# Kernel tuning notes

Measured on AMD Instinct MI355X. Metric: run time of the kernel, lower is better.

Reference implementation:

```python
import jax, jax.numpy as jnp
import numpy as np

N_NODES = 100000
N_EDGES = 3200000
F_IN = 128
NOUT = 32


def _lin(x, W, b):
    return x @ W + b


def _spect_conv(x, src, dst, W, b, n_nodes):
    # edge_attr is all-ones with a single frequency (K=1), so SpectConv reduces to
    # an unweighted scatter-add of linearly transformed source-node features.
    h = x @ W                                   # [N, nout]
    agg = jax.ops.segment_sum(h[src], dst, num_segments=n_nodes)  # [N, nout]
    return agg + b


def setup_inputs() -> dict:
    key = jax.random.key(0)
    ks = jax.random.split(key, 32)
    s = 0.05

    def w(k, shape):
        return jax.random.normal(k, shape, dtype=jnp.float32) * s

    inp = {
        "x": jax.random.normal(ks[0], (N_NODES, F_IN), dtype=jnp.float32),
        "edge_index": jax.random.randint(ks[1], (2, N_EDGES), 0, N_NODES, dtype=jnp.int32),
        # SpectConv weights (single frequency) + biases
        "Wc1": w(ks[2], (F_IN, NOUT)), "bc1": jnp.zeros((NOUT,), jnp.float32),
        "Wc2": w(ks[3], (NOUT, NOUT)), "bc2": jnp.zeros((NOUT,), jnp.float32),
        "Wc3": w(ks[4], (NOUT, NOUT)), "bc3": jnp.zeros((NOUT,), jnp.float32),
        # dense branch weights
        "W11": w(ks[5], (F_IN, NOUT)), "b11": w(ks[6], (NOUT,)),
        "W12": w(ks[7], (F_IN, NOUT)), "b12": w(ks[8], (NOUT,)),
        "W13": w(ks[9], (F_IN, NOUT)), "b13": w(ks[10], (NOUT,)),
        "W21": w(ks[11], (NOUT, NOUT)), "b21": w(ks[12], (NOUT,)),
        "W22": w(ks[13], (NOUT, NOUT)), "b22": w(ks[14], (NOUT,)),
        "W23": w(ks[15], (NOUT, NOUT)), "b23": w(ks[16], (NOUT,)),
        "W31": w(ks[17], (NOUT, NOUT)), "b31": w(ks[18], (NOUT,)),
        "W32": w(ks[19], (NOUT, NOUT)), "b32": w(ks[20], (NOUT,)),
        "W33": w(ks[21], (NOUT, NOUT)), "b33": w(ks[22], (NOUT,)),
        "W2": w(ks[23], (NOUT, 1)), "b2": w(ks[24], (1,)),
    }
    return inp


def reference(x, edge_index,
              Wc1, bc1, Wc2, bc2, Wc3, bc3,
              W11, b11, W12, b12, W13, b13,
              W21, b21, W22, b22, W23, b23,
              W31, b31, W32, b32, W33, b33,
              W2, b2):
    src, dst = edge_index[0], edge_index[1]
    n = x.shape[0]
    relu = jax.nn.relu

    def block(h, Wa, ba, Wc, bc, Wm1, bm1, Wm2, bm2):
        return (relu(_lin(h, Wa, ba))
                + relu(_spect_conv(h, src, dst, Wc, bc, n))
                + relu(_lin(h, Wm1, bm1) * _lin(h, Wm2, bm2)))

    h = block(x, W11, b11, Wc1, bc1, W12, b12, W13, b13)
    h = block(h, W21, b21, Wc2, bc2, W22, b22, W23, b23)
    h = block(h, W31, b31, Wc3, bc3, W32, b32, W33, b33)
    return _lin(h, W2, b2)
```

## Files before the change

### kernel.cpp

```cpp
#include <hip/hip_runtime.h>
#include <hip/hip_bf16.h>

#define N_FEAT 32
#define CBITS 7
#define CAP   6000
#define TILE  8192

typedef __attribute__((ext_vector_type(8))) short short8;
typedef __attribute__((ext_vector_type(4))) float floatx4;

static __device__ __forceinline__ unsigned short f2b(float f) {
    unsigned u = __float_as_uint(f);
    return (unsigned short)((u + 0x7FFFu + ((u >> 16) & 1u)) >> 16);
}
static __device__ __forceinline__ float b2f(unsigned short b) {
    return __uint_as_float(((unsigned)b) << 16);
}

template <int K, bool BF16_IN>
__global__ __launch_bounds__(256)
void transform_mfma_kernel(const void* __restrict__ hin,
                           const float* __restrict__ Wa, const float* __restrict__ ba,
                           const float* __restrict__ Wc,
                           const float* __restrict__ Wm1, const float* __restrict__ bm1,
                           const float* __restrict__ Wm2, const float* __restrict__ bm2,
                           unsigned short* __restrict__ t_pre, unsigned short* __restrict__ t_c,
                           int n_nodes)
{
    constexpr int WPITCH = (K == 32) ? 40 : 136;
    __shared__ unsigned short sW[128][WPITCH];

    const int t = threadIdx.x;
    const int node0 = blockIdx.x * 64;
    const int wave = t >> 6;
    const int lane = t & 63;
    const int m16 = lane & 15;
    const int quad = lane >> 4;

    for (int i = t; i < 128 * K; i += 256) {
        const int c = i & 127, kk = i >> 7;
        const int mat = c >> 5, cl = c & 31;
        const float* W = (mat == 0) ? Wa : (mat == 1) ? Wc : (mat == 2) ? Wm1 : Wm2;
        sW[c][kk] = f2b(W[(size_t)kk * 32 + cl]);
    }
    __syncthreads();

    const int n = node0 + wave * 16 + m16;
    const bool nok = (n < n_nodes);

    floatx4 acc[8];
#pragma unroll
    for (int i = 0; i < 8; ++i) acc[i] = (floatx4){0.f, 0.f, 0.f, 0.f};

#pragma unroll
    for (int k0 = 0; k0 < K; k0 += 32) {
        short8 a;
        if (BF16_IN) {
            const unsigned short* hb = (const unsigned short*)hin;
            a = nok ? *reinterpret_cast<const short8*>(hb + (size_t)n * K + k0 + quad * 8)
                    : (short8){0,0,0,0,0,0,0,0};
        } else {
            const float* hf = (const float*)hin;
            if (nok) {
                const float4 v0 = *reinterpret_cast<const float4*>(hf + (size_t)n * K + k0 + quad * 8);
                const float4 v1 = *reinterpret_cast<const float4*>(hf + (size_t)n * K + k0 + quad * 8 + 4);
                union { short8 v; unsigned short u[8]; } pk;
                pk.u[0] = f2b(v0.x); pk.u[1] = f2b(v0.y); pk.u[2] = f2b(v0.z); pk.u[3] = f2b(v0.w);
                pk.u[4] = f2b(v1.x); pk.u[5] = f2b(v1.y); pk.u[6] = f2b(v1.z); pk.u[7] = f2b(v1.w);
                a = pk.v;
            } else {
                a = (short8){0,0,0,0,0,0,0,0};
            }
        }
#pragma unroll
        for (int t8 = 0; t8 < 8; ++t8) {
            const short8 b = *reinterpret_cast<const short8*>(&sW[t8 * 16 + m16][k0 + quad * 8]);
            acc[t8] = __builtin_amdgcn_mfma_f32_16x16x32_bf16(a, b, acc[t8], 0, 0, 0);
        }
    }

#pragma unroll
    for (int r = 0; r < 4; ++r) {
        const int node = node0 + wave * 16 + quad * 4 + r;
        if (node < n_nodes) {
#pragma unroll
            for (int half = 0; half < 2; ++half) {
                const int c = m16 + half * 16;
                const float av  = acc[0 + half][r] + ba[c];
                const float wcv = acc[2 + half][r];
                const float m1  = acc[4 + half][r] + bm1[c];
                const float m2  = acc[6 + half][r] + bm2[c];
                t_pre[(size_t)node * N_FEAT + c] = f2b(fmaxf(av, 0.f) + fmaxf(m1 * m2, 0.f));
                t_c[(size_t)node * N_FEAT + c] = f2b(wcv);
            }
        }
    }
}

__global__ __launch_bounds__(1024)
void coarse_bin_kernel(const int* __restrict__ src, const int* __restrict__ dst,
                       unsigned* __restrict__ cnt_g, unsigned* __restrict__ binned,
                       int n_edges, int n_buckets)
{
    __shared__ unsigned sorted[TILE];
    __shared__ unsigned short buck[TILE];
    __shared__ unsigned hist[1024];
    __shared__ unsigned lbase[1024];
    __shared__ unsigned gofs[1024];
    __shared__ unsigned wsum[16], woff[16];

    const int t = threadIdx.x;
    const int wave = t >> 6, lane = t & 63;
    const int e0 = blockIdx.x * TILE;
    const int cnt = min(TILE, n_edges - e0);
    if (cnt <= 0) return;

    hist[t] = 0;
    __syncthreads();

    unsigned dv[TILE / 1024], sv[TILE / 1024];
    int nk = 0;
    for (int i = t; i < cnt; i += 1024, ++nk) {
        dv[nk] = (unsigned)dst[e0 + i];
        sv[nk] = (unsigned)src[e0 + i];
        atomicAdd(&hist[dv[nk] >> CBITS], 1u);
    }
    __syncthreads();

    const unsigned myh = hist[t];
    if (t < n_buckets)
        gofs[t] = myh ? atomicAdd(&cnt_g[t], myh) : 0u;

    unsigned v = myh;
#pragma unroll
    for (int off = 1; off < 64; off <<= 1) {
        const unsigned nv = __shfl_up(v, off);
        if (lane >= off) v += nv;
    }
    if (lane == 63) wsum[wave] = v;
    __syncthreads();
    if (t < 16) {
        unsigned s = wsum[t];
#pragma unroll
        for (int off = 1; off < 16; off <<= 1) {
            const unsigned nv = __shfl_up(s, off, 16);
            if (t >= off) s += nv;
        }
        woff[t] = s - wsum[t];
    }
    hist[t] = 0;
    __syncthreads();
    const unsigned lb_mine = v + woff[wave] - myh;
    lbase[t] = lb_mine;
    __syncthreads();

    for (int k = 0; k < nk; ++k) {
        const unsigned b = dv[k] >> CBITS;
        const unsigned pos = lbase[b] + atomicAdd(&hist[b], 1u);
        sorted[pos] = ((dv[k] & ((1u << CBITS) - 1)) << 17) | sv[k];
        buck[pos] = (unsigned short)b;
    }
    __syncthreads();

    for (int p = t; p < cnt; p += 1024) {
        const unsigned b = buck[p];
        const unsigned gp = gofs[b] + ((unsigned)p - lbase[b]);
        if (gp < CAP) binned[(size_t)b * CAP + gp] = sorted[p];
    }
}

__global__ __launch_bounds__(512)
void fine_sort_kernel(const unsigned* __restrict__ binned,
                      const unsigned* __restrict__ cnt_g,
                      unsigned* __restrict__ total_ctr,
                      int* __restrict__ srcs,
                      unsigned* __restrict__ rowstart, unsigned* __restrict__ rowend,
                      int n_nodes, int n_buckets)
{
    __shared__ int sorted_src[CAP];
    __shared__ unsigned hist[512];
    __shared__ unsigned incl[512];
    __shared__ unsigned ebase[512];
    __shared__ unsigned wsum[8], woff[8];
    __shared__ unsigned ob_s;

    const int t = threadIdx.x;
    const int wave = t >> 6, lane = t & 63;
    const int b = blockIdx.x;
    const unsigned cnt = min(cnt_g[b], (unsigned)CAP);
    const int node0 = b << CBITS;
    const int nodes_here = min(128, n_nodes - node0);
    const unsigned* tile = binned + (size_t)b * CAP;

    if (t == 0) ob_s = atomicAdd(total_ctr, cnt);
    hist[t] = 0;
    __syncthreads();
    const unsigned ob = ob_s;

    for (unsigned i = t; i < cnt; i += 512) {
        const unsigned e = tile[i];
        atomicAdd(&hist[((e >> 17) << 2) | ((e & 0x1FFFFu) >> 15)], 1u);
    }
    __syncthreads();

    const unsigned myh = hist[t];
    unsigned v = myh;
#pragma unroll
    for (int off = 1; off < 64; off <<= 1) {
        const unsigned nv = __shfl_up(v, off);
        if (lane >= off) v += nv;
    }
    if (lane == 63) wsum[wave] = v;
    __syncthreads();
    if (t < 8) {
        unsigned s = wsum[t];
#pragma unroll
        for (int off = 1; off < 8; off <<= 1) {
            const unsigned nv = __shfl_up(s, off, 8);
            if (t >= off) s += nv;
        }
        woff[t] = s - wsum[t];
    }
    hist[t] = 0;
    __syncthreads();
    const unsigned my_incl = v + woff[wave];
    incl[t] = my_incl;
    ebase[t] = my_incl - myh;
    __syncthreads();

    if (t < nodes_here) {
        rowstart[node0 + t] = ob + ebase[t << 2];
        rowend[node0 + t]   = ob + incl[(t << 2) + 3];
    }

    for (unsigned i = t; i < cnt; i += 512) {
        const unsigned e = tile[i];
        const unsigned key = ((e >> 17) << 2) | ((e & 0x1FFFFu) >> 15);
        const unsigned pos = ebase[key] + atomicAdd(&hist[key], 1u);
        sorted_src[pos] = (int)(e & 0x1FFFFu);
    }
    __syncthreads();
    for (unsigned i = t; i < cnt; i += 512)
        srcs[ob + i] = sorted_src[i];
}

static __device__ __forceinline__ void add8(float* a, short8 v) {
#pragma unroll
    for (int j = 0; j < 8; ++j) a[j] += b2f((unsigned short)v[j]);
}

__global__ __launch_bounds__(256)
void gather_combine_kernel(const unsigned short* __restrict__ t_c,
                           const unsigned short* __restrict__ t_pre,
                           const unsigned* __restrict__ rowstart,
                           const unsigned* __restrict__ rowend,
                           const int* __restrict__ srcs,
                           const float* __restrict__ bc, unsigned short* __restrict__ hout,
                           int n_nodes)
{
    const int node = blockIdx.x * 64 + (threadIdx.x >> 2);
    const int l4 = threadIdx.x & 3;
    const int f0 = l4 * 8;
    if (node >= n_nodes) return;
    const unsigned lo = rowstart[node], hi = rowend[node];
    float acc[8] = {0.f, 0.f, 0.f, 0.f, 0.f, 0.f, 0.f, 0.f};
    unsigned i = lo;
    for (; i + 8 <= hi; i += 8) {
        short8 v[8];
#pragma unroll
        for (int j = 0; j < 8; ++j)
            v[j] = *reinterpret_cast<const short8*>(t_c + (size_t)srcs[i + j] * N_FEAT + f0);
#pragma unroll
        for (int j = 0; j < 8; ++j) add8(acc, v[j]);
    }
    for (; i + 4 <= hi; i += 4) {
        short8 v[4];
#pragma unroll
        for (int j = 0; j < 4; ++j)
            v[j] = *reinterpret_cast<const short8*>(t_c + (size_t)srcs[i + j] * N_FEAT + f0);
#pragma unroll
        for (int j = 0; j < 4; ++j) add8(acc, v[j]);
    }
    for (; i < hi; ++i)
        add8(acc, *reinterpret_cast<const short8*>(t_c + (size_t)srcs[i] * N_FEAT + f0));

    const short8 p = *reinterpret_cast<const short8*>(t_pre + (size_t)node * N_FEAT + f0);
    union { short8 v; unsigned short u[8]; } r;
#pragma unroll
    for (int j = 0; j < 8; ++j)
        r.u[j] = f2b(b2f((unsigned short)p[j]) + fmaxf(acc[j] + bc[f0 + j], 0.f));
    *reinterpret_cast<short8*>(hout + (size_t)node * N_FEAT + f0) = r.v;
}

__global__ __launch_bounds__(256)
void gather_final_kernel(const unsigned short* __restrict__ t_c,
                         const unsigned short* __restrict__ t_pre,
                         const unsigned* __restrict__ rowstart,
                         const unsigned* __restrict__ rowend,
                         const int* __restrict__ srcs,
                         const float* __restrict__ bc, const float* __restrict__ W2,
                         const float* __restrict__ b2, float* __restrict__ out,
                         int n_nodes)
{
    const int node = blockIdx.x * 64 + (threadIdx.x >> 2);
    const int l4 = threadIdx.x & 3;
    const int f0 = l4 * 8;
    if (node >= n_nodes) return;
    const unsigned lo = rowstart[node], hi = rowend[node];
    float acc[8] = {0.f, 0.f, 0.f, 0.f, 0.f, 0.f, 0.f, 0.f};
    unsigned i = lo;
    for (; i + 8 <= hi; i += 8) {
        short8 v[8];
#pragma unroll
        for (int j = 0; j < 8; ++j)
            v[j] = *reinterpret_cast<const short8*>(t_c + (size_t)srcs[i + j] * N_FEAT + f0);
#pragma unroll
        for (int j = 0; j < 8; ++j) add8(acc, v[j]);
    }
    for (; i + 4 <= hi; i += 4) {
        short8 v[4];
#pragma unroll
        for (int j = 0; j < 4; ++j)
            v[j] = *reinterpret_cast<const short8*>(t_c + (size_t)srcs[i + j] * N_FEAT + f0);
#pragma unroll
        for (int j = 0; j < 4; ++j) add8(acc, v[j]);
    }
    for (; i < hi; ++i)
        add8(acc, *reinterpret_cast<const short8*>(t_c + (size_t)srcs[i] * N_FEAT + f0));

    const short8 p = *reinterpret_cast<const short8*>(t_pre + (size_t)node * N_FEAT + f0);
    float r = 0.f;
#pragma unroll
    for (int j = 0; j < 8; ++j)
        r += (b2f((unsigned short)p[j]) + fmaxf(acc[j] + bc[f0 + j], 0.f)) * W2[f0 + j];
    r += __shfl_down(r, 2, 4);
    r += __shfl_down(r, 1, 4);
    if (l4 == 0) out[node] = r + b2[0];
}

extern "C" void kernel_launch(void* const* d_in, const int* in_sizes, int n_in,
                              void* d_out, int out_size, void* d_ws, size_t ws_size,
                              hipStream_t stream)
{
    const float* x   = (const float*)d_in[0];
    const int*   ei  = (const int*)d_in[1];
    const float* Wc1 = (const float*)d_in[2];  const float* bc1 = (const float*)d_in[3];
    const float* Wc2 = (const float*)d_in[4];  const float* bc2 = (const float*)d_in[5];
    const float* Wc3 = (const float*)d_in[6];  const float* bc3 = (const float*)d_in[7];
    const float* W11 = (const float*)d_in[8];  const float* b11 = (const float*)d_in[9];
    const float* W12 = (const float*)d_in[10]; const float* b12 = (const float*)d_in[11];
    const float* W13 = (const float*)d_in[12]; const float* b13 = (const float*)d_in[13];
    const float* W21 = (const float*)d_in[14]; const float* b21 = (const float*)d_in[15];
    const float* W22 = (const float*)d_in[16]; const float* b22 = (const float*)d_in[17];
    const float* W23 = (const float*)d_in[18]; const float* b23 = (const float*)d_in[19];
    const float* W31 = (const float*)d_in[20]; const float* b31 = (const float*)d_in[21];
    const float* W32 = (const float*)d_in[22]; const float* b32 = (const float*)d_in[23];
    const float* W33 = (const float*)d_in[24]; const float* b33 = (const float*)d_in[25];
    const float* W2  = (const float*)d_in[26]; const float* b2  = (const float*)d_in[27];

    const int n_nodes = in_sizes[0] / 128;
    const int n_edges = in_sizes[1] / 2;
    const int* src = ei;
    const int* dst = ei + n_edges;
    const int n_buckets = (n_nodes + (1 << CBITS) - 1) >> CBITS;

    const size_t feat_elems = (size_t)n_nodes * N_FEAT;

    unsigned short* tpre     = (unsigned short*)d_ws;
    unsigned short* tc       = tpre + feat_elems;
    unsigned short* hbuf     = tc + feat_elems;
    int*            srcs     = (int*)(hbuf + feat_elems);
    unsigned*       rowstart = (unsigned*)(srcs + n_edges);
    unsigned*       rowend   = rowstart + n_nodes;
    unsigned*       cnt_g    = rowend + n_nodes;
    unsigned*       binned   = cnt_g + (n_buckets + 1);

    const int tf_grid = (n_nodes + 63) / 64;
    const int gc_grid = (n_nodes + 63) / 64;
    const int cb_grid = (n_edges + TILE - 1) / TILE;

    hipMemsetAsync(cnt_g, 0, ((size_t)n_buckets + 1) * sizeof(unsigned), stream);
    coarse_bin_kernel<<<cb_grid, 1024, 0, stream>>>(src, dst, cnt_g, binned, n_edges, n_buckets);
    fine_sort_kernel<<<n_buckets, 512, 0, stream>>>(
        binned, cnt_g, cnt_g + n_buckets, srcs, rowstart, rowend, n_nodes, n_buckets);

    transform_mfma_kernel<128, false><<<tf_grid, 256, 0, stream>>>(
        x, W11, b11, Wc1, W12, b12, W13, b13, tpre, tc, n_nodes);
    gather_combine_kernel<<<gc_grid, 256, 0, stream>>>(
        tc, tpre, rowstart, rowend, srcs, bc1, hbuf, n_nodes);

    transform_mfma_kernel<32, true><<<tf_grid, 256, 0, stream>>>(
        hbuf, W21, b21, Wc2, W22, b22, W23, b23, tpre, tc, n_nodes);
    gather_combine_kernel<<<gc_grid, 256, 0, stream>>>(
        tc, tpre, rowstart, rowend, srcs, bc2, hbuf, n_nodes);

    transform_mfma_kernel<32, true><<<tf_grid, 256, 0, stream>>>(
        hbuf, W31, b31, Wc3, W32, b32, W33, b33, tpre, tc, n_nodes);
    gather_final_kernel<<<gc_grid, 256, 0, stream>>>(
        tc, tpre, rowstart, rowend, srcs, bc3, W2, b2, (float*)d_out, n_nodes);
}
```

Before: 342.6 us.

## Split gather feature table into halves to shrink random-access working set

```diff
diff --git a/kernel.cpp b/kernel.cpp
--- a/kernel.cpp
+++ b/kernel.cpp
@@ -24,7 +24,9 @@
                            const float* __restrict__ Wc,
                            const float* __restrict__ Wm1, const float* __restrict__ bm1,
                            const float* __restrict__ Wm2, const float* __restrict__ bm2,
-                           unsigned short* __restrict__ t_pre, unsigned short* __restrict__ t_c,
+                           unsigned short* __restrict__ t_pre,
+                           unsigned short* __restrict__ t_c_lo,
+                           unsigned short* __restrict__ t_c_hi,
                            int n_nodes)
 {
     constexpr int WPITCH = (K == 32) ? 40 : 136;
@@ -91,7 +93,8 @@
                 const float m1  = acc[4 + half][r] + bm1[c];
                 const float m2  = acc[6 + half][r] + bm2[c];
                 t_pre[(size_t)node * N_FEAT + c] = f2b(fmaxf(av, 0.f) + fmaxf(m1 * m2, 0.f));
-                t_c[(size_t)node * N_FEAT + c] = f2b(wcv);
+                if (half == 0) t_c_lo[(size_t)node * 16 + m16] = f2b(wcv);
+                else           t_c_hi[(size_t)node * 16 + m16] = f2b(wcv);
             }
         }
     }
@@ -121,8 +124,8 @@
     unsigned dv[TILE / 1024], sv[TILE / 1024];
     int nk = 0;
     for (int i = t; i < cnt; i += 1024, ++nk) {
-        dv[nk] = (unsigned)dst[e0 + i];
-        sv[nk] = (unsigned)src[e0 + i];
+        dv[nk] = (unsigned)__builtin_nontemporal_load(dst + e0 + i);
+        sv[nk] = (unsigned)__builtin_nontemporal_load(src + e0 + i);
         atomicAdd(&hist[dv[nk] >> CBITS], 1u);
     }
     __syncthreads();
@@ -150,8 +153,7 @@
     }
     hist[t] = 0;
     __syncthreads();
-    const unsigned lb_mine = v + woff[wave] - myh;
-    lbase[t] = lb_mine;
+    lbase[t] = v + woff[wave] - myh;
     __syncthreads();
 
     for (int k = 0; k < nk; ++k) {
@@ -250,92 +252,93 @@
 }
 
 __global__ __launch_bounds__(256)
-void gather_combine_kernel(const unsigned short* __restrict__ t_c,
-                           const unsigned short* __restrict__ t_pre,
-                           const unsigned* __restrict__ rowstart,
-                           const unsigned* __restrict__ rowend,
-                           const int* __restrict__ srcs,
-                           const float* __restrict__ bc, unsigned short* __restrict__ hout,
-                           int n_nodes)
-{
-    const int node = blockIdx.x * 64 + (threadIdx.x >> 2);
-    const int l4 = threadIdx.x & 3;
-    const int f0 = l4 * 8;
+void gather_half_kernel(const unsigned short* __restrict__ t_ch,
+                        const unsigned short* __restrict__ t_pre,
+                        const unsigned* __restrict__ rowstart,
+                        const unsigned* __restrict__ rowend,
+                        const int* __restrict__ srcs,
+                        const float* __restrict__ bc, unsigned short* __restrict__ hout,
+                        int feat_off, int n_nodes)
+{
+    const int node = blockIdx.x * 128 + (threadIdx.x >> 1);
+    const int l2 = threadIdx.x & 1;
+    const int f0 = l2 * 8;
     if (node >= n_nodes) return;
-    const unsigned lo = rowstart[node], hi = rowend[node];
+    const unsigned lo = __builtin_nontemporal_load(rowstart + node);
+    const unsigned hi = __builtin_nontemporal_load(rowend + node);
     float acc[8] = {0.f, 0.f, 0.f, 0.f, 0.f, 0.f, 0.f, 0.f};
     unsigned i = lo;
     for (; i + 8 <= hi; i += 8) {
+        int s[8];
+#pragma unroll
+        for (int j = 0; j < 8; ++j) s[j] = __builtin_nontemporal_load(srcs + i + j);
         short8 v[8];
 #pragma unroll
         for (int j = 0; j < 8; ++j)
-            v[j] = *reinterpret_cast<const short8*>(t_c + (size_t)srcs[i + j] * N_FEAT + f0);
+            v[j] = *reinterpret_cast<const short8*>(t_ch + (size_t)s[j] * 16 + f0);
 #pragma unroll
         for (int j = 0; j < 8; ++j) add8(acc, v[j]);
     }
-    for (; i + 4 <= hi; i += 4) {
-        short8 v[4];
-#pragma unroll
-        for (int j = 0; j < 4; ++j)
-            v[j] = *reinterpret_cast<const short8*>(t_c + (size_t)srcs[i + j] * N_FEAT + f0);
-#pragma unroll
-        for (int j = 0; j < 4; ++j) add8(acc, v[j]);
-    }
-    for (; i < hi; ++i)
-        add8(acc, *reinterpret_cast<const short8*>(t_c + (size_t)srcs[i] * N_FEAT + f0));
-
-    const short8 p = *reinterpret_cast<const short8*>(t_pre + (size_t)node * N_FEAT + f0);
-    union { short8 v; unsigned short u[8]; } r;
+    for (; i < hi; ++i) {
+        const int s = __builtin_nontemporal_load(srcs + i);
+        add8(acc, *reinterpret_cast<const short8*>(t_ch + (size_t)s * 16 + f0));
+    }
+
+    const unsigned short* pp = t_pre + (size_t)node * N_FEAT + feat_off + f0;
+    union { short8 v; unsigned short u[8]; } p, r;
+    p.v = *reinterpret_cast<const short8*>(pp);
 #pragma unroll
     for (int j = 0; j < 8; ++j)
-        r.u[j] = f2b(b2f((unsigned short)p[j]) + fmaxf(acc[j] + bc[f0 + j], 0.f));
-    *reinterpret_cast<short8*>(hout + (size_t)node * N_FEAT + f0) = r.v;
+        r.u[j] = f2b(b2f(p.u[j]) + fmaxf(acc[j] + bc[feat_off + f0 + j], 0.f));
+    *reinterpret_cast<short8*>(hout + (size_t)node * N_FEAT + feat_off + f0) = r.v;
 }
 
 __global__ __launch_bounds__(256)
-void gather_final_kernel(const unsigned short* __restrict__ t_c,
-                         const unsigned short* __restrict__ t_pre,
-                         const unsigned* __restrict__ rowstart,
-                         const unsigned* __restrict__ rowend,
-                         const int* __restrict__ srcs,
-                         const float* __restrict__ bc, const float* __restrict__ W2,
-                         const float* __restrict__ b2, float* __restrict__ out,
-                         int n_nodes)
-{
-    const int node = blockIdx.x * 64 + (threadIdx.x >> 2);
-    const int l4 = threadIdx.x & 3;
-    const int f0 = l4 * 8;
+void gather_final_half_kernel(const unsigned short* __restrict__ t_ch,
+                              const unsigned short* __restrict__ t_pre,
+                              const unsigned* __restrict__ rowstart,
+                              const unsigned* __restrict__ rowend,
+                              const int* __restrict__ srcs,
+                              const float* __restrict__ bc, const float* __restrict__ W2,
+                              const float* __restrict__ b2, float* __restrict__ out,
+                              int feat_off, int n_nodes)
+{
+    const int node = blockIdx.x * 128 + (threadIdx.x >> 1);
+    const int l2 = threadIdx.x & 1;
+    const int f0 = l2 * 8;
     if (node >= n_nodes) return;
-    const unsigned lo = rowstart[node], hi = rowend[node];
+    const unsigned lo = __builtin_nontemporal_load(rowstart + node);
+    const unsigned hi = __builtin_nontemporal_load(rowend + node);
     float acc[8] = {0.f, 0.f, 0.f, 0.f, 0.f, 0.f, 0.f, 0.f};
     unsigned i = lo;
     for (; i + 8 <= hi; i += 8) {
+        int s[8];
+#pragma unroll
+        for (int j = 0; j < 8; ++j) s[j] = __builtin_nontemporal_load(srcs + i + j);
         short8 v[8];
 #pragma unroll
         for (int j = 0; j < 8; ++j)
-            v[j] = *reinterpret_cast<const short8*>(t_c + (size_t)srcs[i + j] * N_FEAT + f0);
+            v[j] = *reinterpret_cast<const short8*>(t_ch + (size_t)s[j] * 16 + f0);
 #pragma unroll
         for (int j = 0; j < 8; ++j) add8(acc, v[j]);
     }
-    for (; i + 4 <= hi; i += 4) {
-        short8 v[4];
-#pragma unroll
-        for (int j = 0; j < 4; ++j)
-            v[j] = *reinterpret_cast<const short8*>(t_c + (size_t)srcs[i + j] * N_FEAT + f0);
-#pragma unroll
-        for (int j = 0; j < 4; ++j) add8(acc, v[j]);
-    }
-    for (; i < hi; ++i)
-        add8(acc, *reinterpret_cast<const short8*>(t_c + (size_t)srcs[i] * N_FEAT + f0));
-
-    const short8 p = *reinterpret_cast<const short8*>(t_pre + (size_t)node * N_FEAT + f0);
+    for (; i < hi; ++i) {
+        const int s = __builtin_nontemporal_load(srcs + i);
+        add8(acc, *reinterpret_cast<const short8*>(t_ch + (size_t)s * 16 + f0));
+    }
+
+    const unsigned short* pp = t_pre + (size_t)node * N_FEAT + feat_off + f0;
+    union { short8 v; unsigned short u[8]; } p;
+    p.v = *reinterpret_cast<const short8*>(pp);
     float r = 0.f;
 #pragma unroll
     for (int j = 0; j < 8; ++j)
-        r += (b2f((unsigned short)p[j]) + fmaxf(acc[j] + bc[f0 + j], 0.f)) * W2[f0 + j];
-    r += __shfl_down(r, 2, 4);
-    r += __shfl_down(r, 1, 4);
-    if (l4 == 0) out[node] = r + b2[0];
+        r += (b2f(p.u[j]) + fmaxf(acc[j] + bc[feat_off + f0 + j], 0.f)) * W2[feat_off + f0 + j];
+    r += __shfl_down(r, 1, 2);
+    if (l2 == 0) {
+        if (feat_off == 0) out[node] = r + b2[0];
+        else               out[node] += r;
+    }
 }
 
 extern "C" void kernel_launch(void* const* d_in, const int* in_sizes, int n_in,
@@ -365,10 +368,12 @@
     const int n_buckets = (n_nodes + (1 << CBITS) - 1) >> CBITS;
 
     const size_t feat_elems = (size_t)n_nodes * N_FEAT;
+    const size_t half_elems = (size_t)n_nodes * 16;
 
     unsigned short* tpre     = (unsigned short*)d_ws;
-    unsigned short* tc       = tpre + feat_elems;
-    unsigned short* hbuf     = tc + feat_elems;
+    unsigned short* tclo     = tpre + feat_elems;
+    unsigned short* tchi     = tclo + half_elems;
+    unsigned short* hbuf     = tchi + half_elems;
     int*            srcs     = (int*)(hbuf + feat_elems);
     unsigned*       rowstart = (unsigned*)(srcs + n_edges);
     unsigned*       rowend   = rowstart + n_nodes;
@@ -376,7 +381,7 @@
     unsigned*       binned   = cnt_g + (n_buckets + 1);
 
     const int tf_grid = (n_nodes + 63) / 64;
-    const int gc_grid = (n_nodes + 63) / 64;
+    const int gh_grid = (n_nodes + 127) / 128;
     const int cb_grid = (n_edges + TILE - 1) / TILE;
 
     hipMemsetAsync(cnt_g, 0, ((size_t)n_buckets + 1) * sizeof(unsigned), stream);
@@ -385,17 +390,23 @@
         binned, cnt_g, cnt_g + n_buckets, srcs, rowstart, rowend, n_nodes, n_buckets);
 
     transform_mfma_kernel<128, false><<<tf_grid, 256, 0, stream>>>(
-        x, W11, b11, Wc1, W12, b12, W13, b13, tpre, tc, n_nodes);
-    gather_combine_kernel<<<gc_grid, 256, 0, stream>>>(
-        tc, tpre, rowstart, rowend, srcs, bc1, hbuf, n_nodes);
+        x, W11, b11, Wc1, W12, b12, W13, b13, tpre, tclo, tchi, n_nodes);
+    gather_half_kernel<<<gh_grid, 256, 0, stream>>>(
+        tclo, tpre, rowstart, rowend, srcs, bc1, hbuf, 0, n_nodes);
+    gather_half_kernel<<<gh_grid, 256, 0, stream>>>(
+        tchi, tpre, rowstart, rowend, srcs, bc1, hbuf, 16, n_nodes);
 
     transform_mfma_kernel<32, true><<<tf_grid, 256, 0, stream>>>(
-        hbuf, W21, b21, Wc2, W22, b22, W23, b23, tpre, tc, n_nodes);
-    gather_combine_kernel<<<gc_grid, 256, 0, stream>>>(
-        tc, tpre, rowstart, rowend, srcs, bc2, hbuf, n_nodes);
+        hbuf, W21, b21, Wc2, W22, b22, W23, b23, tpre, tclo, tchi, n_nodes);
+    gather_half_kernel<<<gh_grid, 256, 0, stream>>>(
+        tclo, tpre, rowstart, rowend, srcs, bc2, hbuf, 0, n_nodes);
+    gather_half_kernel<<<gh_grid, 256, 0, stream>>>(
+        tchi, tpre, rowstart, rowend, srcs, bc2, hbuf, 16, n_nodes);
 
     transform_mfma_kernel<32, true><<<tf_grid, 256, 0, stream>>>(
-        hbuf, W31, b31, Wc3, W32, b32, W33, b33, tpre, tc, n_nodes);
-    gather_final_kernel<<<gc_grid, 256, 0, stream>>>(
-        tc, tpre, rowstart, rowend, srcs, bc3, W2, b2, (float*)d_out, n_nodes);
-}
+        hbuf, W31, b31, Wc3, W32, b32, W33, b33, tpre, tclo, tchi, n_nodes);
+    gather_final_half_kernel<<<gh_grid, 256, 0, stream>>>(
+        tclo, tpre, rowstart, rowend, srcs, bc3, W2, b2, (float*)d_out, 0, n_nodes);
+    gather_final_half_kernel<<<gh_grid, 256, 0, stream>>>(
+        tchi, tpre, rowstart, rowend, srcs, bc3, W2, b2, (float*)d_out, 16, n_nodes);
+}
```

Result: slower. 468.3 us (+36.7%).

## Gather by source-quartile ranges with block barriers; nontemporal index loads

Applied to the files above, without the earlier changes.

```diff
diff --git a/kernel.cpp b/kernel.cpp
--- a/kernel.cpp
+++ b/kernel.cpp
@@ -121,8 +121,8 @@
     unsigned dv[TILE / 1024], sv[TILE / 1024];
     int nk = 0;
     for (int i = t; i < cnt; i += 1024, ++nk) {
-        dv[nk] = (unsigned)dst[e0 + i];
-        sv[nk] = (unsigned)src[e0 + i];
+        dv[nk] = (unsigned)__builtin_nontemporal_load(dst + e0 + i);
+        sv[nk] = (unsigned)__builtin_nontemporal_load(src + e0 + i);
         atomicAdd(&hist[dv[nk] >> CBITS], 1u);
     }
     __syncthreads();
@@ -150,8 +150,7 @@
     }
     hist[t] = 0;
     __syncthreads();
-    const unsigned lb_mine = v + woff[wave] - myh;
-    lbase[t] = lb_mine;
+    lbase[t] = v + woff[wave] - myh;
     __syncthreads();
 
     for (int k = 0; k < nk; ++k) {
@@ -174,7 +173,7 @@
                       const unsigned* __restrict__ cnt_g,
                       unsigned* __restrict__ total_ctr,
                       int* __restrict__ srcs,
-                      unsigned* __restrict__ rowstart, unsigned* __restrict__ rowend,
+                      unsigned* __restrict__ qstart, unsigned* __restrict__ rowend,
                       int n_nodes, int n_buckets)
 {
     __shared__ int sorted_src[CAP];
@@ -229,8 +228,10 @@
     __syncthreads();
 
     if (t < nodes_here) {
-        rowstart[node0 + t] = ob + ebase[t << 2];
-        rowend[node0 + t]   = ob + incl[(t << 2) + 3];
+#pragma unroll
+        for (int q = 0; q < 4; ++q)
+            qstart[(size_t)(node0 + t) * 4 + q] = ob + ebase[(t << 2) + q];
+        rowend[node0 + t] = ob + incl[(t << 2) + 3];
     }
 
     for (unsigned i = t; i < cnt; i += 512) {
@@ -249,10 +250,32 @@
     for (int j = 0; j < 8; ++j) a[j] += b2f((unsigned short)v[j]);
 }
 
+static __device__ __forceinline__ void gather_range(
+    float* acc, const unsigned short* __restrict__ t_c,
+    const int* __restrict__ srcs, unsigned lo, unsigned hi, int f0)
+{
+    unsigned i = lo;
+    for (; i + 8 <= hi; i += 8) {
+        int s[8];
+#pragma unroll
+        for (int j = 0; j < 8; ++j) s[j] = __builtin_nontemporal_load(srcs + i + j);
+        short8 v[8];
+#pragma unroll
+        for (int j = 0; j < 8; ++j)
+            v[j] = *reinterpret_cast<const short8*>(t_c + (size_t)s[j] * N_FEAT + f0);
+#pragma unroll
+        for (int j = 0; j < 8; ++j) add8(acc, v[j]);
+    }
+    for (; i < hi; ++i) {
+        const int s = __builtin_nontemporal_load(srcs + i);
+        add8(acc, *reinterpret_cast<const short8*>(t_c + (size_t)s * N_FEAT + f0));
+    }
+}
+
 __global__ __launch_bounds__(256)
 void gather_combine_kernel(const unsigned short* __restrict__ t_c,
                            const unsigned short* __restrict__ t_pre,
-                           const unsigned* __restrict__ rowstart,
+                           const unsigned* __restrict__ qstart,
                            const unsigned* __restrict__ rowend,
                            const int* __restrict__ srcs,
                            const float* __restrict__ bc, unsigned short* __restrict__ hout,
@@ -261,41 +284,34 @@
     const int node = blockIdx.x * 64 + (threadIdx.x >> 2);
     const int l4 = threadIdx.x & 3;
     const int f0 = l4 * 8;
-    if (node >= n_nodes) return;
-    const unsigned lo = rowstart[node], hi = rowend[node];
+    const bool ok = (node < n_nodes);
+    uint4 qs = ok ? *reinterpret_cast<const uint4*>(qstart + (size_t)node * 4)
+                  : (uint4){0, 0, 0, 0};
+    const unsigned qe = ok ? rowend[node] : 0u;
     float acc[8] = {0.f, 0.f, 0.f, 0.f, 0.f, 0.f, 0.f, 0.f};
-    unsigned i = lo;
-    for (; i + 8 <= hi; i += 8) {
-        short8 v[8];
-#pragma unroll
-        for (int j = 0; j < 8; ++j)
-            v[j] = *reinterpret_cast<const short8*>(t_c + (size_t)srcs[i + j] * N_FEAT + f0);
-#pragma unroll
-        for (int j = 0; j < 8; ++j) add8(acc, v[j]);
-    }
-    for (; i + 4 <= hi; i += 4) {
-        short8 v[4];
-#pragma unroll
-        for (int j = 0; j < 4; ++j)
-            v[j] = *reinterpret_cast<const short8*>(t_c + (size_t)srcs[i + j] * N_FEAT + f0);
-#pragma unroll
-        for (int j = 0; j < 4; ++j) add8(acc, v[j]);
-    }
-    for (; i < hi; ++i)
-        add8(acc, *reinterpret_cast<const short8*>(t_c + (size_t)srcs[i] * N_FEAT + f0));
-
+
+    if (ok) gather_range(acc, t_c, srcs, qs.x, qs.y, f0);
+    __syncthreads();
+    if (ok) gather_range(acc, t_c, srcs, qs.y, qs.z, f0);
+    __syncthreads();
+    if (ok) gather_range(acc, t_c, srcs, qs.z, qs.w, f0);
+    __syncthreads();
+    if (ok) gather_range(acc, t_c, srcs, qs.w, qe, f0);
+
+    if (!ok) return;
     const short8 p = *reinterpret_cast<const short8*>(t_pre + (size_t)node * N_FEAT + f0);
-    union { short8 v; unsigned short u[8]; } r;
+    union { short8 v; unsigned short u[8]; } pr, r;
+    pr.v = p;
 #pragma unroll
     for (int j = 0; j < 8; ++j)
-        r.u[j] = f2b(b2f((unsigned short)p[j]) + fmaxf(acc[j] + bc[f0 + j], 0.f));
+        r.u[j] = f2b(b2f(pr.u[j]) + fmaxf(acc[j] + bc[f0 + j], 0.f));
     *reinterpret_cast<short8*>(hout + (size_t)node * N_FEAT + f0) = r.v;
 }
 
 __global__ __launch_bounds__(256)
 void gather_final_kernel(const unsigned short* __restrict__ t_c,
                          const unsigned short* __restrict__ t_pre,
-                         const unsigned* __restrict__ rowstart,
+                         const unsigned* __restrict__ qstart,
                          const unsigned* __restrict__ rowend,
                          const int* __restrict__ srcs,
                          const float* __restrict__ bc, const float* __restrict__ W2,
@@ -305,34 +321,28 @@
     const int node = blockIdx.x * 64 + (threadIdx.x >> 2);
     const int l4 = threadIdx.x & 3;
     const int f0 = l4 * 8;
-    if (node >= n_nodes) return;
-    const unsigned lo = rowstart[node], hi = rowend[node];
+    const bool ok = (node < n_nodes);
+    uint4 qs = ok ? *reinterpret_cast<const uint4*>(qstart + (size_t)node * 4)
+                  : (uint4){0, 0, 0, 0};
+    const unsigned qe = ok ? rowend[node] : 0u;
     float acc[8] = {0.f, 0.f, 0.f, 0.f, 0.f, 0.f, 0.f, 0.f};
-    unsigned i = lo;
-    for (; i + 8 <= hi; i += 8) {
-        short8 v[8];
-#pragma unroll
-        for (int j = 0; j < 8; ++j)
-            v[j] = *reinterpret_cast<const short8*>(t_c + (size_t)srcs[i + j] * N_FEAT + f0);
-#pragma unroll
-        for (int j = 0; j < 8; ++j) add8(acc, v[j]);
-    }
-    for (; i + 4 <= hi; i += 4) {
-        short8 v[4];
-#pragma unroll
-        for (int j = 0; j < 4; ++j)
-            v[j] = *reinterpret_cast<const short8*>(t_c + (size_t)srcs[i + j] * N_FEAT + f0);
-#pragma unroll
-        for (int j = 0; j < 4; ++j) add8(acc, v[j]);
-    }
-    for (; i < hi; ++i)
-        add8(acc, *reinterpret_cast<const short8*>(t_c + (size_t)srcs[i] * N_FEAT + f0));
-
+
+    if (ok) gather_range(acc, t_c, srcs, qs.x, qs.y, f0);
+    __syncthreads();
+    if (ok) gather_range(acc, t_c, srcs, qs.y, qs.z, f0);
+    __syncthreads();
+    if (ok) gather_range(acc, t_c, srcs, qs.z, qs.w, f0);
+    __syncthreads();
+    if (ok) gather_range(acc, t_c, srcs, qs.w, qe, f0);
+
+    if (!ok) return;
     const short8 p = *reinterpret_cast<const short8*>(t_pre + (size_t)node * N_FEAT + f0);
+    union { short8 v; unsigned short u[8]; } pr;
+    pr.v = p;
     float r = 0.f;
 #pragma unroll
     for (int j = 0; j < 8; ++j)
-        r += (b2f((unsigned short)p[j]) + fmaxf(acc[j] + bc[f0 + j], 0.f)) * W2[f0 + j];
+        r += (b2f(pr.u[j]) + fmaxf(acc[j] + bc[f0 + j], 0.f)) * W2[f0 + j];
     r += __shfl_down(r, 2, 4);
     r += __shfl_down(r, 1, 4);
     if (l4 == 0) out[node] = r + b2[0];
@@ -366,14 +376,14 @@
 
     const size_t feat_elems = (size_t)n_nodes * N_FEAT;
 
-    unsigned short* tpre     = (unsigned short*)d_ws;
-    unsigned short* tc       = tpre + feat_elems;
-    unsigned short* hbuf     = tc + feat_elems;
-    int*            srcs     = (int*)(hbuf + feat_elems);
-    unsigned*       rowstart = (unsigned*)(srcs + n_edges);
-    unsigned*       rowend   = rowstart + n_nodes;
-    unsigned*       cnt_g    = rowend + n_nodes;
-    unsigned*       binned   = cnt_g + (n_buckets + 1);
+    unsigned short* tpre   = (unsigned short*)d_ws;
+    unsigned short* tc     = tpre + feat_elems;
+    unsigned short* hbuf   = tc + feat_elems;
+    int*            srcs   = (int*)(hbuf + feat_elems);
+    unsigned*       qstart = (unsigned*)(srcs + n_edges);
+    unsigned*       rowend = qstart + (size_t)n_nodes * 4;
+    unsigned*       cnt_g  = rowend + n_nodes;
+    unsigned*       binned = cnt_g + (n_buckets + 1);
 
     const int tf_grid = (n_nodes + 63) / 64;
     const int gc_grid = (n_nodes + 63) / 64;
@@ -382,20 +392,20 @@
     hipMemsetAsync(cnt_g, 0, ((size_t)n_buckets + 1) * sizeof(unsigned), stream);
     coarse_bin_kernel<<<cb_grid, 1024, 0, stream>>>(src, dst, cnt_g, binned, n_edges, n_buckets);
     fine_sort_kernel<<<n_buckets, 512, 0, stream>>>(
-        binned, cnt_g, cnt_g + n_buckets, srcs, rowstart, rowend, n_nodes, n_buckets);
+        binned, cnt_g, cnt_g + n_buckets, srcs, qstart, rowend, n_nodes, n_buckets);
 
     transform_mfma_kernel<128, false><<<tf_grid, 256, 0, stream>>>(
         x, W11, b11, Wc1, W12, b12, W13, b13, tpre, tc, n_nodes);
     gather_combine_kernel<<<gc_grid, 256, 0, stream>>>(
-        tc, tpre, rowstart, rowend, srcs, bc1, hbuf, n_nodes);
+        tc, tpre, qstart, rowend, srcs, bc1, hbuf, n_nodes);
 
     transform_mfma_kernel<32, true><<<tf_grid, 256, 0, stream>>>(
         hbuf, W21, b21, Wc2, W22, b22, W23, b23, tpre, tc, n_nodes);
     gather_combine_kernel<<<gc_grid, 256, 0, stream>>>(
-        tc, tpre, rowstart, rowend, srcs, bc2, hbuf, n_nodes);
+        tc, tpre, qstart, rowend, srcs, bc2, hbuf, n_nodes);
 
     transform_mfma_kernel<32, true><<<tf_grid, 256, 0, stream>>>(
         hbuf, W31, b31, Wc3, W32, b32, W33, b33, tpre, tc, n_nodes);
     gather_final_kernel<<<gc_grid, 256, 0, stream>>>(
-        tc, tpre, rowstart, rowend, srcs, bc3, W2, b2, (float*)d_out, n_nodes);
-}
+        tc, tpre, qstart, rowend, srcs, bc3, W2, b2, (float*)d_out, n_nodes);
+}
```

Result: slower. 435.8 us (+27.2%).

## Fuse gather-combine with next layer's MFMA transform and ping-pong feature buffers

Applied to the files above, without the earlier changes.

```diff
diff --git a/kernel.cpp b/kernel.cpp
--- a/kernel.cpp
+++ b/kernel.cpp
@@ -17,18 +17,17 @@
     return __uint_as_float(((unsigned)b) << 16);
 }
 
-template <int K, bool BF16_IN>
 __global__ __launch_bounds__(256)
-void transform_mfma_kernel(const void* __restrict__ hin,
-                           const float* __restrict__ Wa, const float* __restrict__ ba,
-                           const float* __restrict__ Wc,
-                           const float* __restrict__ Wm1, const float* __restrict__ bm1,
-                           const float* __restrict__ Wm2, const float* __restrict__ bm2,
-                           unsigned short* __restrict__ t_pre, unsigned short* __restrict__ t_c,
-                           int n_nodes)
-{
-    constexpr int WPITCH = (K == 32) ? 40 : 136;
-    __shared__ unsigned short sW[128][WPITCH];
+void transform128_kernel(const float* __restrict__ x,
+                         const float* __restrict__ Wa, const float* __restrict__ ba,
+                         const float* __restrict__ Wc,
+                         const float* __restrict__ Wm1, const float* __restrict__ bm1,
+                         const float* __restrict__ Wm2, const float* __restrict__ bm2,
+                         unsigned short* __restrict__ t_pre, unsigned short* __restrict__ t_c,
+                         int n_nodes)
+{
+    constexpr int K = 128;
+    __shared__ unsigned short sW[128][136];
 
     const int t = threadIdx.x;
     const int node0 = blockIdx.x * 64;
@@ -55,22 +54,15 @@
 #pragma unroll
     for (int k0 = 0; k0 < K; k0 += 32) {
         short8 a;
-        if (BF16_IN) {
-            const unsigned short* hb = (const unsigned short*)hin;
-            a = nok ? *reinterpret_cast<const short8*>(hb + (size_t)n * K + k0 + quad * 8)
-                    : (short8){0,0,0,0,0,0,0,0};
+        if (nok) {
+            const float4 v0 = *reinterpret_cast<const float4*>(x + (size_t)n * K + k0 + quad * 8);
+            const float4 v1 = *reinterpret_cast<const float4*>(x + (size_t)n * K + k0 + quad * 8 + 4);
+            union { short8 v; unsigned short u[8]; } pk;
+            pk.u[0] = f2b(v0.x); pk.u[1] = f2b(v0.y); pk.u[2] = f2b(v0.z); pk.u[3] = f2b(v0.w);
+            pk.u[4] = f2b(v1.x); pk.u[5] = f2b(v1.y); pk.u[6] = f2b(v1.z); pk.u[7] = f2b(v1.w);
+            a = pk.v;
         } else {
-            const float* hf = (const float*)hin;
-            if (nok) {
-                const float4 v0 = *reinterpret_cast<const float4*>(hf + (size_t)n * K + k0 + quad * 8);
-                const float4 v1 = *reinterpret_cast<const float4*>(hf + (size_t)n * K + k0 + quad * 8 + 4);
-                union { short8 v; unsigned short u[8]; } pk;
-                pk.u[0] = f2b(v0.x); pk.u[1] = f2b(v0.y); pk.u[2] = f2b(v0.z); pk.u[3] = f2b(v0.w);
-                pk.u[4] = f2b(v1.x); pk.u[5] = f2b(v1.y); pk.u[6] = f2b(v1.z); pk.u[7] = f2b(v1.w);
-                a = pk.v;
-            } else {
-                a = (short8){0,0,0,0,0,0,0,0};
-            }
+            a = (short8){0,0,0,0,0,0,0,0};
         }
 #pragma unroll
         for (int t8 = 0; t8 < 8; ++t8) {
@@ -121,8 +113,8 @@
     unsigned dv[TILE / 1024], sv[TILE / 1024];
     int nk = 0;
     for (int i = t; i < cnt; i += 1024, ++nk) {
-        dv[nk] = (unsigned)dst[e0 + i];
-        sv[nk] = (unsigned)src[e0 + i];
+        dv[nk] = (unsigned)__builtin_nontemporal_load(dst + e0 + i);
+        sv[nk] = (unsigned)__builtin_nontemporal_load(src + e0 + i);
         atomicAdd(&hist[dv[nk] >> CBITS], 1u);
     }
     __syncthreads();
@@ -150,8 +142,7 @@
     }
     hist[t] = 0;
     __syncthreads();
-    const unsigned lb_mine = v + woff[wave] - myh;
-    lbase[t] = lb_mine;
+    lbase[t] = v + woff[wave] - myh;
     __syncthreads();
 
     for (int k = 0; k < nk; ++k) {
@@ -249,47 +240,109 @@
     for (int j = 0; j < 8; ++j) a[j] += b2f((unsigned short)v[j]);
 }
 
-__global__ __launch_bounds__(256)
-void gather_combine_kernel(const unsigned short* __restrict__ t_c,
-                           const unsigned short* __restrict__ t_pre,
-                           const unsigned* __restrict__ rowstart,
-                           const unsigned* __restrict__ rowend,
-                           const int* __restrict__ srcs,
-                           const float* __restrict__ bc, unsigned short* __restrict__ hout,
-                           int n_nodes)
-{
-    const int node = blockIdx.x * 64 + (threadIdx.x >> 2);
-    const int l4 = threadIdx.x & 3;
-    const int f0 = l4 * 8;
-    if (node >= n_nodes) return;
-    const unsigned lo = rowstart[node], hi = rowend[node];
-    float acc[8] = {0.f, 0.f, 0.f, 0.f, 0.f, 0.f, 0.f, 0.f};
+static __device__ __forceinline__ void gather_row(
+    float* acc, const unsigned short* __restrict__ t_c,
+    const int* __restrict__ srcs, unsigned lo, unsigned hi, int f0)
+{
     unsigned i = lo;
     for (; i + 8 <= hi; i += 8) {
+        int s[8];
+#pragma unroll
+        for (int j = 0; j < 8; ++j) s[j] = __builtin_nontemporal_load(srcs + i + j);
         short8 v[8];
 #pragma unroll
         for (int j = 0; j < 8; ++j)
-            v[j] = *reinterpret_cast<const short8*>(t_c + (size_t)srcs[i + j] * N_FEAT + f0);
+            v[j] = *reinterpret_cast<const short8*>(t_c + (size_t)s[j] * N_FEAT + f0);
 #pragma unroll
         for (int j = 0; j < 8; ++j) add8(acc, v[j]);
     }
-    for (; i + 4 <= hi; i += 4) {
-        short8 v[4];
-#pragma unroll
-        for (int j = 0; j < 4; ++j)
-            v[j] = *reinterpret_cast<const short8*>(t_c + (size_t)srcs[i + j] * N_FEAT + f0);
-#pragma unroll
-        for (int j = 0; j < 4; ++j) add8(acc, v[j]);
-    }
-    for (; i < hi; ++i)
-        add8(acc, *reinterpret_cast<const short8*>(t_c + (size_t)srcs[i] * N_FEAT + f0));
-
-    const short8 p = *reinterpret_cast<const short8*>(t_pre + (size_t)node * N_FEAT + f0);
-    union { short8 v; unsigned short u[8]; } r;
-#pragma unroll
-    for (int j = 0; j < 8; ++j)
-        r.u[j] = f2b(b2f((unsigned short)p[j]) + fmaxf(acc[j] + bc[f0 + j], 0.f));
-    *reinterpret_cast<short8*>(hout + (size_t)node * N_FEAT + f0) = r.v;
+    for (; i < hi; ++i) {
+        const int s = __builtin_nontemporal_load(srcs + i);
+        add8(acc, *reinterpret_cast<const short8*>(t_c + (size_t)s * N_FEAT + f0));
+    }
+}
+
+__global__ __launch_bounds__(256)
+void gather_transform_kernel(const unsigned short* __restrict__ t_c_in,
+                             const unsigned short* __restrict__ t_pre_in,
+                             const unsigned* __restrict__ rowstart,
+                             const unsigned* __restrict__ rowend,
+                             const int* __restrict__ srcs,
+                             const float* __restrict__ bc,
+                             const float* __restrict__ Wa, const float* __restrict__ ba,
+                             const float* __restrict__ Wc,
+                             const float* __restrict__ Wm1, const float* __restrict__ bm1,
+                             const float* __restrict__ Wm2, const float* __restrict__ bm2,
+                             unsigned short* __restrict__ t_pre_out,
+                             unsigned short* __restrict__ t_c_out,
+                             int n_nodes)
+{
+    __shared__ unsigned short sW[128][40];
+    __shared__ unsigned short sH[64][40];
+
+    const int t = threadIdx.x;
+    const int node0 = blockIdx.x * 64;
+
+    for (int i = t; i < 128 * 32; i += 256) {
+        const int c = i & 127, kk = i >> 7;
+        const int mat = c >> 5, cl = c & 31;
+        const float* W = (mat == 0) ? Wa : (mat == 1) ? Wc : (mat == 2) ? Wm1 : Wm2;
+        sW[c][kk] = f2b(W[(size_t)kk * 32 + cl]);
+    }
+
+    const int gnode = node0 + (t >> 2);
+    const int l4 = t & 3;
+    const int f0 = l4 * 8;
+    if (gnode < n_nodes) {
+        const unsigned lo = __builtin_nontemporal_load(rowstart + gnode);
+        const unsigned hi = __builtin_nontemporal_load(rowend + gnode);
+        float acc[8] = {0.f, 0.f, 0.f, 0.f, 0.f, 0.f, 0.f, 0.f};
+        gather_row(acc, t_c_in, srcs, lo, hi, f0);
+
+        const short8 p = *reinterpret_cast<const short8*>(t_pre_in + (size_t)gnode * N_FEAT + f0);
+        union { short8 v; unsigned short u[8]; } pr;
+        pr.v = p;
+#pragma unroll
+        for (int j = 0; j < 8; ++j)
+            sH[t >> 2][f0 + j] = f2b(b2f(pr.u[j]) + fmaxf(acc[j] + bc[f0 + j], 0.f));
+    } else {
+#pragma unroll
+        for (int j = 0; j < 8; ++j) sH[t >> 2][f0 + j] = 0;
+    }
+    __syncthreads();
+
+    const int wave = t >> 6;
+    const int lane = t & 63;
+    const int m16 = lane & 15;
+    const int quad = lane >> 4;
+
+    floatx4 acc2[8];
+#pragma unroll
+    for (int i = 0; i < 8; ++i) acc2[i] = (floatx4){0.f, 0.f, 0.f, 0.f};
+
+    const short8 a = *reinterpret_cast<const short8*>(&sH[wave * 16 + m16][quad * 8]);
+#pragma unroll
+    for (int t8 = 0; t8 < 8; ++t8) {
+        const short8 b = *reinterpret_cast<const short8*>(&sW[t8 * 16 + m16][quad * 8]);
+        acc2[t8] = __builtin_amdgcn_mfma_f32_16x16x32_bf16(a, b, acc2[t8], 0, 0, 0);
+    }
+
+#pragma unroll
+    for (int r = 0; r < 4; ++r) {
+        const int node = node0 + wave * 16 + quad * 4 + r;
+        if (node < n_nodes) {
+#pragma unroll
+            for (int half = 0; half < 2; ++half) {
+                const int c = m16 + half * 16;
+                const float av  = acc2[0 + half][r] + ba[c];
+                const float wcv = acc2[2 + half][r];
+                const float m1  = acc2[4 + half][r] + bm1[c];
+                const float m2  = acc2[6 + half][r] + bm2[c];
+                t_pre_out[(size_t)node * N_FEAT + c] = f2b(fmaxf(av, 0.f) + fmaxf(m1 * m2, 0.f));
+                t_c_out[(size_t)node * N_FEAT + c] = f2b(wcv);
+            }
+        }
+    }
 }
 
 __global__ __launch_bounds__(256)
@@ -306,33 +359,18 @@
     const int l4 = threadIdx.x & 3;
     const int f0 = l4 * 8;
     if (node >= n_nodes) return;
-    const unsigned lo = rowstart[node], hi = rowend[node];
+    const unsigned lo = __builtin_nontemporal_load(rowstart + node);
+    const unsigned hi = __builtin_nontemporal_load(rowend + node);
     float acc[8] = {0.f, 0.f, 0.f, 0.f, 0.f, 0.f, 0.f, 0.f};
-    unsigned i = lo;
-    for (; i + 8 <= hi; i += 8) {
-        short8 v[8];
-#pragma unroll
-        for (int j = 0; j < 8; ++j)
-            v[j] = *reinterpret_cast<const short8*>(t_c + (size_t)srcs[i + j] * N_FEAT + f0);
-#pragma unroll
-        for (int j = 0; j < 8; ++j) add8(acc, v[j]);
-    }
-    for (; i + 4 <= hi; i += 4) {
-        short8 v[4];
-#pragma unroll
-        for (int j = 0; j < 4; ++j)
-            v[j] = *reinterpret_cast<const short8*>(t_c + (size_t)srcs[i + j] * N_FEAT + f0);
-#pragma unroll
-        for (int j = 0; j < 4; ++j) add8(acc, v[j]);
-    }
-    for (; i < hi; ++i)
-        add8(acc, *reinterpret_cast<const short8*>(t_c + (size_t)srcs[i] * N_FEAT + f0));
+    gather_row(acc, t_c, srcs, lo, hi, f0);
 
     const short8 p = *reinterpret_cast<const short8*>(t_pre + (size_t)node * N_FEAT + f0);
+    union { short8 v; unsigned short u[8]; } pr;
+    pr.v = p;
     float r = 0.f;
 #pragma unroll
     for (int j = 0; j < 8; ++j)
-        r += (b2f((unsigned short)p[j]) + fmaxf(acc[j] + bc[f0 + j], 0.f)) * W2[f0 + j];
+        r += (b2f(pr.u[j]) + fmaxf(acc[j] + bc[f0 + j], 0.f)) * W2[f0 + j];
     r += __shfl_down(r, 2, 4);
     r += __shfl_down(r, 1, 4);
     if (l4 == 0) out[node] = r + b2[0];
@@ -366,10 +404,11 @@
 
     const size_t feat_elems = (size_t)n_nodes * N_FEAT;
 
-    unsigned short* tpre     = (unsigned short*)d_ws;
-    unsigned short* tc       = tpre + feat_elems;
-    unsigned short* hbuf     = tc + feat_elems;
-    int*            srcs     = (int*)(hbuf + feat_elems);
+    unsigned short* tpreA    = (unsigned short*)d_ws;
+    unsigned short* tcA      = tpreA + feat_elems;
+    unsigned short* tpreB    = tcA + feat_elems;
+    unsigned short* tcB      = tpreB + feat_elems;
+    int*            srcs     = (int*)(tcB + feat_elems);
     unsigned*       rowstart = (unsigned*)(srcs + n_edges);
     unsigned*       rowend   = rowstart + n_nodes;
     unsigned*       cnt_g    = rowend + n_nodes;
@@ -384,18 +423,17 @@
     fine_sort_kernel<<<n_buckets, 512, 0, stream>>>(
         binned, cnt_g, cnt_g + n_buckets, srcs, rowstart, rowend, n_nodes, n_buckets);
 
-    transform_mfma_kernel<128, false><<<tf_grid, 256, 0, stream>>>(
-        x, W11, b11, Wc1, W12, b12, W13, b13, tpre, tc, n_nodes);
-    gather_combine_kernel<<<gc_grid, 256, 0, stream>>>(
-        tc, tpre, rowstart, rowend, srcs, bc1, hbuf, n_nodes);
-
-    transform_mfma_kernel<32, true><<<tf_grid, 256, 0, stream>>>(
-        hbuf, W21, b21, Wc2, W22, b22, W23, b23, tpre, tc, n_nodes);
-    gather_combine_kernel<<<gc_grid, 256, 0, stream>>>(
-        tc, tpre, rowstart, rowend, srcs, bc2, hbuf, n_nodes);
-
-    transform_mfma_kernel<32, true><<<tf_grid, 256, 0, stream>>>(
-        hbuf, W31, b31, Wc3, W32, b32, W33, b33, tpre, tc, n_nodes);
+    transform128_kernel<<<tf_grid, 256, 0, stream>>>(
+        x, W11, b11, Wc1, W12, b12, W13, b13, tpreA, tcA, n_nodes);
+
+    gather_transform_kernel<<<gc_grid, 256, 0, stream>>>(
+        tcA, tpreA, rowstart, rowend, srcs, bc1,
+        W21, b21, Wc2, W22, b22, W23, b23, tpreB, tcB, n_nodes);
+
+    gather_transform_kernel<<<gc_grid, 256, 0, stream>>>(
+        tcB, tpreB, rowstart, rowend, srcs, bc2,
+        W31, b31, Wc3, W32, b32, W33, b33, tpreA, tcA, n_nodes);
+
     gather_final_kernel<<<gc_grid, 256, 0, stream>>>(
-        tc, tpre, rowstart, rowend, srcs, bc3, W2, b2, (float*)d_out, n_nodes);
-}
+        tcA, tpreA, rowstart, rowend, srcs, bc3, W2, b2, (float*)d_out, n_nodes);
+}
```

New measurement: 358.6 us. 4.7% more time.
